# Kernel optimization log

Hardware: AMD Instinct MI355X
Metric: run time of the kernel (lower is better)

The kernel has to match this reference:

```python
import jax, jax.numpy as jnp
import numpy as np

B, N, P, C, H = 8, 512, 16, 512, 8
HD = C // H  # 64


def setup_inputs() -> dict:
    key = jax.random.key(0)
    k1, k2, k3, k4, k5 = jax.random.split(key, 5)
    x = jax.random.normal(k1, (B, N, P, C), dtype=jnp.float32)
    # binary observation mask; force slot 0 valid so masked mean never divides by 0
    mask = (jax.random.uniform(k2, (B, N, P)) > 0.3).astype(jnp.float32)
    mask = mask.at[:, :, 0].set(1.0)
    lens = jax.random.randint(k3, (B,), 1, N)
    lens_mask = jnp.ones((B, N), dtype=jnp.float32)
    # parameters (torch Linear stored as [in, out] here; qkv_bias=False, proj has bias)
    Wqkv = jax.random.normal(k4, (C, 3 * C), dtype=jnp.float32) * (1.0 / np.sqrt(C))
    Wproj = jax.random.normal(k5, (C, C), dtype=jnp.float32) * (1.0 / np.sqrt(C))
    bproj = jnp.zeros((C,), dtype=jnp.float32)
    return {"x": x, "mask": mask, "lens": lens, "lens_mask": lens_mask,
            "Wqkv": Wqkv, "Wproj": Wproj, "bproj": bproj}


def reference(x, mask, lens, lens_mask, Wqkv, Wproj, bproj):
    # lens / lens_mask are unused by the original forward
    b, n, p, c = x.shape
    h, hd = H, c // H
    qkv = jnp.einsum('bnpc,cd->bnpd', x, Wqkv).reshape(b, n, p, 3, h, hd)
    # q: take P-slot 0                       -> [B,H,N,hd]
    q = qkv[:, :, 0, 0].transpose(0, 2, 1, 3)
    # k: masked mean over P                  -> [B,H,N,hd]
    m = mask[..., None, None]                      # [B,N,P,1,1]
    k = (jnp.where(m > 0, qkv[:, :, :, 1], 0.0).sum(axis=2) / m.sum(axis=2))
    k = k.transpose(0, 2, 1, 3)
    # v: pack P into channel dim             -> [B,H,N,hd*P]
    v = qkv[:, :, :, 2].transpose(0, 3, 1, 4, 2).reshape(b, h, n, hd * p)
    # SDPA over N (scale by 1/sqrt(head_dim of q))
    scale = 1.0 / np.sqrt(hd)
    attn = jax.nn.softmax(jnp.einsum('bhnd,bhmd->bhnm', q, k) * scale, axis=-1)
    out = jnp.einsum('bhnm,bhme->bhne', attn, v)            # [B,H,N,hd*P]
    # unpack P back out                       -> [B,N,P,C]
    out = out.reshape(b, h, n, hd, p).transpose(0, 2, 4, 1, 3).reshape(b, n, p, c)
    return out @ Wproj + bproj
```

## Files before the change

### kernel.cpp

```cpp
#include <hip/hip_runtime.h>

typedef _Float16 f16;
typedef __attribute__((ext_vector_type(8))) _Float16 half8;
typedef __attribute__((ext_vector_type(2))) _Float16 half2v;
typedef __attribute__((ext_vector_type(4))) float float4v;

#define MODE_QK 0
#define MODE_V 1
#define MODE_PV 2
#define MODE_PROJ 3


__device__ __forceinline__ void gload16(const f16* g, f16* l) {
    __builtin_amdgcn_global_load_lds(
        (const __attribute__((address_space(1))) void*)g,
        (__attribute__((address_space(3))) void*)l, 16, 0, 0);
}

__global__ __launch_bounds__(256) void prep_kernel(
    const float* __restrict__ x, const float* __restrict__ mask,
    const float* __restrict__ Wqkv, const float* __restrict__ Wproj,
    f16* __restrict__ xf, f16* __restrict__ xmean,
    f16* __restrict__ WT, f16* __restrict__ WpT)
{
    if (blockIdx.x >= 4096) {
        int idx = (blockIdx.x - 4096) * 256 + threadIdx.x;
        if (idx < 1536 * 512) {
            int d = idx >> 9, c = idx & 511;
            WT[idx] = (f16)Wqkv[c * 1536 + d];
        } else {
            int i2 = idx - 1536 * 512;
            int d = i2 >> 9, c = i2 & 511;
            WpT[i2] = (f16)Wproj[c * 512 + d];
        }
        return;
    }
    int bn = blockIdx.x;
    int t = threadIdx.x;
    const float* xrow = x + (size_t)bn * 16 * 512;
    const float* mrow = mask + (size_t)bn * 16;
    float msum = 0.f;
    #pragma unroll
    for (int p = 0; p < 16; p++) msum += mrow[p];
    int c = t * 2;
    float a0 = 0.f, a1 = 0.f;
    #pragma unroll
    for (int p = 0; p < 16; p++) {
        float2 v = *(const float2*)(xrow + p * 512 + c);
        float m = mrow[p];
        a0 += m * v.x; a1 += m * v.y;
        half2v h; h[0] = (f16)v.x; h[1] = (f16)v.y;
        *(half2v*)(xf + (size_t)bn * 16 * 512 + p * 512 + c) = h;
    }
    float inv = 1.f / msum;
    half2v hm; hm[0] = (f16)(a0 * inv); hm[1] = (f16)(a1 * inv);
    *(half2v*)(xmean + (size_t)bn * 512 + c) = hm;
}

template<int MODE>
__global__ __launch_bounds__(256) void gemm128(
    const f16* __restrict__ pA, const f16* __restrict__ pA2,
    const f16* __restrict__ pB,
    f16* __restrict__ outa, f16* __restrict__ outb,
    float* __restrict__ outf, const float* __restrict__ bias)
{
    __shared__ __align__(16) f16 sm[18432];
    const int t = threadIdx.x;
    const int lane = t & 63;
    const int w = t >> 6;
    const int wm = w & 1, wn = w >> 1;
    const int quad = lane >> 4, l15 = lane & 15;

    const int n0 = blockIdx.x * 128;
    const int m0 = blockIdx.y * 128;
    int vb = 0, vp = 0, z = 0;

    const f16* Abase; size_t sA;
    const f16* Bbase; size_t sB;
    if constexpr (MODE == MODE_QK) {
        if (n0 < 512) { Abase = pA;  sA = 8192; }
        else          { Abase = pA2; sA = 512;  }
        Bbase = pB; sB = 512;
    } else if constexpr (MODE == MODE_V) {
        z = blockIdx.z; vb = z >> 4; vp = z & 15;
        Abase = pA; sA = 512;
        Bbase = pB + ((size_t)vb * 512 * 16 + vp) * 512; sB = 8192;
    } else if constexpr (MODE == MODE_PV) {
        z = blockIdx.z;
        Abase = pA + (size_t)z * 512 * 512; sA = 512;
        Bbase = pB + (size_t)z * 1024 * 512; sB = 512;
    } else {
        Abase = pA; sA = 512;
        Bbase = pB; sB = 512;
    }

    const int rlo = (lane >> 2), kof = (lane & 3) * 8;
    const f16* ga0 = Abase + (size_t)(m0 + w * 16 + rlo) * sA + kof;
    const f16* ga1 = Abase + (size_t)(m0 + (w + 4) * 16 + rlo) * sA + kof;
    const f16* gb0 = Bbase + (size_t)(n0 + w * 16 + rlo) * sB + kof;
    const f16* gb1 = Bbase + (size_t)(n0 + (w + 4) * 16 + rlo) * sB + kof;

    float4v acc[4][4];
    #pragma unroll
    for (int i = 0; i < 4; i++)
        #pragma unroll
        for (int j = 0; j < 4; j++)
            acc[i][j] = (float4v){0.f, 0.f, 0.f, 0.f};

    {
        f16* d = sm;
        gload16(ga0, d + w * 512); gload16(ga1, d + (w + 4) * 512);
        gload16(gb0, d + 4096 + w * 512); gload16(gb1, d + 4096 + (w + 4) * 512);
        ga0 += 32; ga1 += 32; gb0 += 32; gb1 += 32;
    }
    int cur = 0;
    for (int kt = 0; kt < 16; kt++) {
        __syncthreads();
        if (kt < 15) {
            f16* d = sm + (cur ^ 1) * 8192;
            gload16(ga0, d + w * 512); gload16(ga1, d + (w + 4) * 512);
            gload16(gb0, d + 4096 + w * 512); gload16(gb1, d + 4096 + (w + 4) * 512);
            ga0 += 32; ga1 += 32; gb0 += 32; gb1 += 32;
        }
        const f16* Asr = sm + cur * 8192;
        const f16* Bsr = Asr + 4096;
        half8 af[4], bf[4];
        #pragma unroll
        for (int mi = 0; mi < 4; mi++)
            af[mi] = *(const half8*)&Asr[(wm * 64 + mi * 16 + l15) * 32 + quad * 8];
        #pragma unroll
        for (int ni = 0; ni < 4; ni++)
            bf[ni] = *(const half8*)&Bsr[(wn * 64 + ni * 16 + l15) * 32 + quad * 8];
        #pragma unroll
        for (int mi = 0; mi < 4; mi++)
            #pragma unroll
            for (int ni = 0; ni < 4; ni++)
                acc[mi][ni] = __builtin_amdgcn_mfma_f32_16x16x32_f16(
                    af[mi], bf[ni], acc[mi][ni], 0, 0, 0);
        cur ^= 1;
    }

    __syncthreads();

    if constexpr (MODE == MODE_PROJ) {
        float* pwf = (float*)sm + w * 2176;
        const int rr4 = lane >> 4, c4 = (lane & 15) * 4;
        float4v bb = *(const float4v*)&bias[n0 + wn * 64 + c4];
        #pragma unroll
        for (int c2 = 0; c2 < 2; c2++) {
            #pragma unroll
            for (int mh = 0; mh < 2; mh++) {
                int mi = c2 * 2 + mh;
                #pragma unroll
                for (int ni = 0; ni < 4; ni++)
                    #pragma unroll
                    for (int i = 0; i < 4; i++)
                        pwf[(mh * 16 + quad * 4 + i) * 68 + ni * 16 + l15] =
                            acc[mi][ni][i];
            }
            #pragma unroll
            for (int s = 0; s < 8; s++) {
                int r = s * 4 + rr4;
                float4v v = *(const float4v*)&pwf[r * 68 + c4];
                *(float4v*)&outf[(size_t)(m0 + wm * 64 + c2 * 32 + r) * 512 +
                                 n0 + wn * 64 + c4] = v + bb;
            }
        }
    } else {
        f16* pw = sm + w * 4608;
        #pragma unroll
        for (int mi = 0; mi < 4; mi++)
            #pragma unroll
            for (int ni = 0; ni < 4; ni++)
                #pragma unroll
                for (int i = 0; i < 4; i++)
                    pw[(mi * 16 + quad * 4 + i) * 72 + ni * 16 + l15] =
                        (f16)acc[mi][ni][i];
        const int rr8 = lane >> 3, c8 = (lane & 7) * 8;
        #pragma unroll
        for (int s = 0; s < 8; s++) {
            int r = s * 8 + rr8;
            half8 v = *(const half8*)&pw[r * 72 + c8];
            int gr = m0 + wm * 64 + r;
            int gc = n0 + wn * 64 + c8;
            if constexpr (MODE == MODE_QK) {
                int b = gr >> 9, n = gr & 511;
                if (gc < 512)
                    *(half8*)&outa[(((size_t)(b * 8 + (gc >> 6))) * 512 + n) * 64 + (gc & 63)] = v;
                else {
                    int jj = gc - 512;
                    *(half8*)&outb[(((size_t)(b * 8 + (jj >> 6))) * 512 + n) * 64 + (jj & 63)] = v;
                }
            } else if constexpr (MODE == MODE_V) {
                int h = gr >> 6, dd = gr & 63;
                *(half8*)&outa[(((size_t)(vb * 8 + h)) * 1024 + vp * 64 + dd) * 512 + gc] = v;
            } else {
                int p = gc >> 6, dd = gc & 63;
                int b = z >> 3, h = z & 7;
                *(half8*)&outa[((size_t)(b * 512 + gr) * 16 + p) * 512 + h * 64 + dd] = v;
            }
        }
    }
}

__global__ __launch_bounds__(256) void qk_softmax_kernel(
    const f16* __restrict__ q, const f16* __restrict__ k, f16* __restrict__ Pout)
{
    __shared__ __align__(16) f16 sm[16896];
    const int t = threadIdx.x;
    const int lane = t & 63, w = t >> 6;
    const int quad = lane >> 4, l15 = lane & 15;
    const int bh = blockIdx.y;
    const int n0 = blockIdx.x * 64;

    const f16* kbase = k + (size_t)bh * 512 * 64;
    const f16* qp = q + ((size_t)bh * 512 + n0 + w * 16 + l15) * 64 + quad * 8;
    half8 a0 = *(const half8*)qp;
    half8 a1 = *(const half8*)(qp + 32);

    float4v acc[32];
    #pragma unroll
    for (int f = 0; f < 32; f++) acc[f] = (float4v){0.f, 0.f, 0.f, 0.f};

    const int srow = lane >> 3, scol = lane & 7;
    #pragma unroll
    for (int c = 0; c < 4; c++) {
        __syncthreads();
        #pragma unroll
        for (int i = 0; i < 4; i++) {
            int ci2 = w * 4 + i;
            int row = ci2 * 8 + srow;
            gload16(kbase + c * 8192 + row * 64 + ((scol ^ (row & 7)) << 3),
                    sm + ci2 * 512 + lane * 8);
        }
        __syncthreads();
        #pragma unroll
        for (int fl = 0; fl < 8; fl++) {
            int row16 = fl * 16 + l15;
            int sw = row16 & 7;
            half8 b0 = *(const half8*)&sm[row16 * 64 + ((quad ^ sw) << 3)];
            half8 b1 = *(const half8*)&sm[row16 * 64 + (((quad + 4) ^ sw) << 3)];
            acc[c * 8 + fl] = __builtin_amdgcn_mfma_f32_16x16x32_f16(
                a0, b0, acc[c * 8 + fl], 0, 0, 0);
            acc[c * 8 + fl] = __builtin_amdgcn_mfma_f32_16x16x32_f16(
                a1, b1, acc[c * 8 + fl], 0, 0, 0);
        }
    }

    float mx0 = -3e38f, mx1 = -3e38f, mx2 = -3e38f, mx3 = -3e38f;
    #pragma unroll
    for (int f = 0; f < 32; f++) {
        mx0 = fmaxf(mx0, acc[f][0]); mx1 = fmaxf(mx1, acc[f][1]);
        mx2 = fmaxf(mx2, acc[f][2]); mx3 = fmaxf(mx3, acc[f][3]);
    }
    #pragma unroll
    for (int off = 1; off < 16; off <<= 1) {
        mx0 = fmaxf(mx0, __shfl_xor(mx0, off));
        mx1 = fmaxf(mx1, __shfl_xor(mx1, off));
        mx2 = fmaxf(mx2, __shfl_xor(mx2, off));
        mx3 = fmaxf(mx3, __shfl_xor(mx3, off));
    }
    float s0 = 0.f, s1 = 0.f, s2 = 0.f, s3 = 0.f;
    #pragma unroll
    for (int f = 0; f < 32; f++) {
        float e0 = __expf(0.125f * (acc[f][0] - mx0));
        float e1 = __expf(0.125f * (acc[f][1] - mx1));
        float e2 = __expf(0.125f * (acc[f][2] - mx2));
        float e3 = __expf(0.125f * (acc[f][3] - mx3));
        acc[f][0] = e0; acc[f][1] = e1; acc[f][2] = e2; acc[f][3] = e3;
        s0 += e0; s1 += e1; s2 += e2; s3 += e3;
    }
    #pragma unroll
    for (int off = 1; off < 16; off <<= 1) {
        s0 += __shfl_xor(s0, off);
        s1 += __shfl_xor(s1, off);
        s2 += __shfl_xor(s2, off);
        s3 += __shfl_xor(s3, off);
    }
    float r0 = 1.f / s0, r1 = 1.f / s1, r2 = 1.f / s2, r3 = 1.f / s3;

    __syncthreads();
    f16* pb = sm + w * 4224;
    const int rr = lane >> 2, cb = (lane & 3) * 64;
    #pragma unroll
    for (int cc = 0; cc < 2; cc++) {
        #pragma unroll
        for (int ff = 0; ff < 16; ff++) {
            int f = cc * 16 + ff;
            pb[(quad * 4 + 0) * 264 + ff * 16 + l15] = (f16)(acc[f][0] * r0);
            pb[(quad * 4 + 1) * 264 + ff * 16 + l15] = (f16)(acc[f][1] * r1);
            pb[(quad * 4 + 2) * 264 + ff * 16 + l15] = (f16)(acc[f][2] * r2);
            pb[(quad * 4 + 3) * 264 + ff * 16 + l15] = (f16)(acc[f][3] * r3);
        }
        size_t gb = ((size_t)bh * 512 + n0 + w * 16 + rr) * 512 + cc * 256 + cb;
        #pragma unroll
        for (int s = 0; s < 8; s++) {
            half8 v = *(const half8*)&pb[rr * 264 + cb + s * 8];
            *(half8*)&Pout[gb + s * 8] = v;
        }
    }
}

extern "C" void kernel_launch(void* const* d_in, const int* in_sizes, int n_in,
                              void* d_out, int out_size, void* d_ws, size_t ws_size,
                              hipStream_t stream)
{
    (void)in_sizes; (void)n_in; (void)out_size; (void)ws_size;
    const float* x     = (const float*)d_in[0];
    const float* mask  = (const float*)d_in[1];
    const float* Wqkv  = (const float*)d_in[4];
    const float* Wproj = (const float*)d_in[5];
    const float* bproj = (const float*)d_in[6];
    float* out = (float*)d_out;
    char* ws = (char*)d_ws;

    f16* xf16  = (f16*)(ws + 0);
    f16* vT    = (f16*)(ws + 67108864);
    f16* xmean = (f16*)(ws + 134217728);
    f16* WT    = (f16*)(ws + 138412032);
    f16* WpT   = (f16*)(ws + 139984896);
    f16* qb    = (f16*)(ws + 140509184);
    f16* kb    = (f16*)(ws + 144703488);
    f16* Pm    = (f16*)(ws + 148897792);
    f16* ypre  = xf16;

    prep_kernel<<<dim3(8192), dim3(256), 0, stream>>>(
        x, mask, Wqkv, Wproj, xf16, xmean, WT, WpT);
    gemm128<MODE_QK><<<dim3(8, 32), dim3(256), 0, stream>>>(
        xf16, xmean, WT, qb, kb, nullptr, nullptr);
    gemm128<MODE_V><<<dim3(4, 4, 128), dim3(256), 0, stream>>>(
        WT + 1024 * 512, nullptr, xf16, vT, nullptr, nullptr, nullptr);
    qk_softmax_kernel<<<dim3(8, 64), dim3(256), 0, stream>>>(qb, kb, Pm);
    gemm128<MODE_PV><<<dim3(8, 4, 64), dim3(256), 0, stream>>>(
        Pm, nullptr, vT, ypre, nullptr, nullptr, nullptr);
    gemm128<MODE_PROJ><<<dim3(4, 512), dim3(256), 0, stream>>>(
        ypre, nullptr, WpT, nullptr, nullptr, out, bproj);
}
```

Measured before the change: 438.6 us.

## Remap GEMM blocks per XCD, swizzle LDS tiles, shrink epilogue staging

Block indices in the GEMM and QK-softmax kernels are flattened to 1D and remapped so that consecutive logical tiles go to the same XCD chiplet. This aims to improve L2 reuse of shared A/B panels. The LDS tile layout gets an XOR swizzle on the k-offset, applied on both the global-to-LDS copy and the fragment reads, to cut bank conflicts. The epilogue staging is split into smaller chunks, which lowers shared memory from 36KB to 32KB to raise occupancy, at the cost of more passes through LDS.

```diff
diff --git a/kernel.cpp b/kernel.cpp
--- a/kernel.cpp
+++ b/kernel.cpp
@@ -57,23 +57,29 @@
     *(half2v*)(xmean + (size_t)bn * 512 + c) = hm;
 }
 
-template<int MODE>
+template<int MODE, int NXB, int NYB>
 __global__ __launch_bounds__(256) void gemm128(
     const f16* __restrict__ pA, const f16* __restrict__ pA2,
     const f16* __restrict__ pB,
     f16* __restrict__ outa, f16* __restrict__ outb,
     float* __restrict__ outf, const float* __restrict__ bias)
 {
-    __shared__ __align__(16) f16 sm[18432];
+    __shared__ __align__(16) f16 sm[16384];
     const int t = threadIdx.x;
     const int lane = t & 63;
     const int w = t >> 6;
     const int wm = w & 1, wn = w >> 1;
     const int quad = lane >> 4, l15 = lane & 15;
 
-    const int n0 = blockIdx.x * 128;
-    const int m0 = blockIdx.y * 128;
-    int vb = 0, vp = 0, z = 0;
+    const int chunk = (int)gridDim.x >> 3;
+    const int L = ((int)blockIdx.x & 7) * chunk + ((int)blockIdx.x >> 3);
+    const int xb = L & ((1 << NXB) - 1);
+    const int rest = L >> NXB;
+    const int yb = rest & ((1 << NYB) - 1);
+    const int z = rest >> NYB;
+    const int n0 = xb * 128;
+    const int m0 = yb * 128;
+    int vb = 0, vp = 0;
 
     const f16* Abase; size_t sA;
     const f16* Bbase; size_t sB;
@@ -82,11 +88,10 @@
         else          { Abase = pA2; sA = 512;  }
         Bbase = pB; sB = 512;
     } else if constexpr (MODE == MODE_V) {
-        z = blockIdx.z; vb = z >> 4; vp = z & 15;
+        vb = z >> 4; vp = z & 15;
         Abase = pA; sA = 512;
         Bbase = pB + ((size_t)vb * 512 * 16 + vp) * 512; sB = 8192;
     } else if constexpr (MODE == MODE_PV) {
-        z = blockIdx.z;
         Abase = pA + (size_t)z * 512 * 512; sA = 512;
         Bbase = pB + (size_t)z * 1024 * 512; sB = 512;
     } else {
@@ -94,7 +99,8 @@
         Bbase = pB; sB = 512;
     }
 
-    const int rlo = (lane >> 2), kof = (lane & 3) * 8;
+    const int rlo = (lane >> 2);
+    const int kof = (((lane & 3) ^ ((rlo >> 1) & 3)) * 8);
     const f16* ga0 = Abase + (size_t)(m0 + w * 16 + rlo) * sA + kof;
     const f16* ga1 = Abase + (size_t)(m0 + (w + 4) * 16 + rlo) * sA + kof;
     const f16* gb0 = Bbase + (size_t)(n0 + w * 16 + rlo) * sB + kof;
@@ -113,6 +119,7 @@
         gload16(gb0, d + 4096 + w * 512); gload16(gb1, d + 4096 + (w + 4) * 512);
         ga0 += 32; ga1 += 32; gb0 += 32; gb1 += 32;
     }
+    const int sws = (l15 >> 1) & 3;
     int cur = 0;
     for (int kt = 0; kt < 16; kt++) {
         __syncthreads();
@@ -127,10 +134,12 @@
         half8 af[4], bf[4];
         #pragma unroll
         for (int mi = 0; mi < 4; mi++)
-            af[mi] = *(const half8*)&Asr[(wm * 64 + mi * 16 + l15) * 32 + quad * 8];
+            af[mi] = *(const half8*)&Asr[(wm * 64 + mi * 16 + l15) * 32 +
+                                         ((quad ^ sws) * 8)];
         #pragma unroll
         for (int ni = 0; ni < 4; ni++)
-            bf[ni] = *(const half8*)&Bsr[(wn * 64 + ni * 16 + l15) * 32 + quad * 8];
+            bf[ni] = *(const half8*)&Bsr[(wn * 64 + ni * 16 + l15) * 32 +
+                                         ((quad ^ sws) * 8)];
         #pragma unroll
         for (int mi = 0; mi < 4; mi++)
             #pragma unroll
@@ -143,61 +152,61 @@
     __syncthreads();
 
     if constexpr (MODE == MODE_PROJ) {
-        float* pwf = (float*)sm + w * 2176;
-        const int rr4 = lane >> 4, c4 = (lane & 15) * 4;
-        float4v bb = *(const float4v*)&bias[n0 + wn * 64 + c4];
-        #pragma unroll
-        for (int c2 = 0; c2 < 2; c2++) {
+        float* pwf = (float*)sm + w * 1088;
+        const int rr4 = lane >> 4, c4c = (lane & 15) * 4;
+        float4v bb = *(const float4v*)&bias[n0 + wn * 64 + c4c];
+        #pragma unroll
+        for (int mi = 0; mi < 4; mi++) {
+            #pragma unroll
+            for (int ni = 0; ni < 4; ni++)
+                #pragma unroll
+                for (int i = 0; i < 4; i++)
+                    pwf[(quad * 4 + i) * 68 + ni * 16 + l15] = acc[mi][ni][i];
+            #pragma unroll
+            for (int s = 0; s < 4; s++) {
+                int r = s * 4 + rr4;
+                float4v v = *(const float4v*)&pwf[r * 68 + c4c];
+                *(float4v*)&outf[(size_t)(m0 + wm * 64 + mi * 16 + r) * 512 +
+                                 n0 + wn * 64 + c4c] = v + bb;
+            }
+        }
+    } else {
+        f16* pw = sm + w * 2304;
+        const int rr8 = lane >> 3, c8 = (lane & 7) * 8;
+        #pragma unroll
+        for (int hf = 0; hf < 2; hf++) {
             #pragma unroll
             for (int mh = 0; mh < 2; mh++) {
-                int mi = c2 * 2 + mh;
+                int mi = hf * 2 + mh;
                 #pragma unroll
                 for (int ni = 0; ni < 4; ni++)
                     #pragma unroll
                     for (int i = 0; i < 4; i++)
-                        pwf[(mh * 16 + quad * 4 + i) * 68 + ni * 16 + l15] =
-                            acc[mi][ni][i];
+                        pw[(mh * 16 + quad * 4 + i) * 72 + ni * 16 + l15] =
+                            (f16)acc[mi][ni][i];
             }
             #pragma unroll
-            for (int s = 0; s < 8; s++) {
-                int r = s * 4 + rr4;
-                float4v v = *(const float4v*)&pwf[r * 68 + c4];
-                *(float4v*)&outf[(size_t)(m0 + wm * 64 + c2 * 32 + r) * 512 +
-                                 n0 + wn * 64 + c4] = v + bb;
-            }
-        }
-    } else {
-        f16* pw = sm + w * 4608;
-        #pragma unroll
-        for (int mi = 0; mi < 4; mi++)
-            #pragma unroll
-            for (int ni = 0; ni < 4; ni++)
-                #pragma unroll
-                for (int i = 0; i < 4; i++)
-                    pw[(mi * 16 + quad * 4 + i) * 72 + ni * 16 + l15] =
-                        (f16)acc[mi][ni][i];
-        const int rr8 = lane >> 3, c8 = (lane & 7) * 8;
-        #pragma unroll
-        for (int s = 0; s < 8; s++) {
-            int r = s * 8 + rr8;
-            half8 v = *(const half8*)&pw[r * 72 + c8];
-            int gr = m0 + wm * 64 + r;
-            int gc = n0 + wn * 64 + c8;
-            if constexpr (MODE == MODE_QK) {
-                int b = gr >> 9, n = gr & 511;
-                if (gc < 512)
-                    *(half8*)&outa[(((size_t)(b * 8 + (gc >> 6))) * 512 + n) * 64 + (gc & 63)] = v;
-                else {
-                    int jj = gc - 512;
-                    *(half8*)&outb[(((size_t)(b * 8 + (jj >> 6))) * 512 + n) * 64 + (jj & 63)] = v;
+            for (int s = 0; s < 4; s++) {
+                int r = s * 8 + rr8;
+                half8 v = *(const half8*)&pw[r * 72 + c8];
+                int gr = m0 + wm * 64 + hf * 32 + r;
+                int gc = n0 + wn * 64 + c8;
+                if constexpr (MODE == MODE_QK) {
+                    int b = gr >> 9, n = gr & 511;
+                    if (gc < 512)
+                        *(half8*)&outa[(((size_t)(b * 8 + (gc >> 6))) * 512 + n) * 64 + (gc & 63)] = v;
+                    else {
+                        int jj = gc - 512;
+                        *(half8*)&outb[(((size_t)(b * 8 + (jj >> 6))) * 512 + n) * 64 + (jj & 63)] = v;
+                    }
+                } else if constexpr (MODE == MODE_V) {
+                    int h = gr >> 6, dd = gr & 63;
+                    *(half8*)&outa[(((size_t)(vb * 8 + h)) * 1024 + vp * 64 + dd) * 512 + gc] = v;
+                } else {
+                    int p = gc >> 6, dd = gc & 63;
+                    int b = z >> 3, h = z & 7;
+                    *(half8*)&outa[((size_t)(b * 512 + gr) * 16 + p) * 512 + h * 64 + dd] = v;
                 }
-            } else if constexpr (MODE == MODE_V) {
-                int h = gr >> 6, dd = gr & 63;
-                *(half8*)&outa[(((size_t)(vb * 8 + h)) * 1024 + vp * 64 + dd) * 512 + gc] = v;
-            } else {
-                int p = gc >> 6, dd = gc & 63;
-                int b = z >> 3, h = z & 7;
-                *(half8*)&outa[((size_t)(b * 512 + gr) * 16 + p) * 512 + h * 64 + dd] = v;
             }
         }
     }
@@ -210,8 +219,9 @@
     const int t = threadIdx.x;
     const int lane = t & 63, w = t >> 6;
     const int quad = lane >> 4, l15 = lane & 15;
-    const int bh = blockIdx.y;
-    const int n0 = blockIdx.x * 64;
+    const int L = ((int)blockIdx.x & 7) * 64 + ((int)blockIdx.x >> 3);
+    const int bh = L >> 3;
+    const int n0 = (L & 7) * 64;
 
     const f16* kbase = k + (size_t)bh * 512 * 64;
     const f16* qp = q + ((size_t)bh * 512 + n0 + w * 16 + l15) * 64 + quad * 8;
@@ -326,13 +336,13 @@
 
     prep_kernel<<<dim3(8192), dim3(256), 0, stream>>>(
         x, mask, Wqkv, Wproj, xf16, xmean, WT, WpT);
-    gemm128<MODE_QK><<<dim3(8, 32), dim3(256), 0, stream>>>(
+    gemm128<MODE_QK, 3, 5><<<dim3(256), dim3(256), 0, stream>>>(
         xf16, xmean, WT, qb, kb, nullptr, nullptr);
-    gemm128<MODE_V><<<dim3(4, 4, 128), dim3(256), 0, stream>>>(
+    gemm128<MODE_V, 2, 2><<<dim3(2048), dim3(256), 0, stream>>>(
         WT + 1024 * 512, nullptr, xf16, vT, nullptr, nullptr, nullptr);
-    qk_softmax_kernel<<<dim3(8, 64), dim3(256), 0, stream>>>(qb, kb, Pm);
-    gemm128<MODE_PV><<<dim3(8, 4, 64), dim3(256), 0, stream>>>(
+    qk_softmax_kernel<<<dim3(512), dim3(256), 0, stream>>>(qb, kb, Pm);
+    gemm128<MODE_PV, 3, 2><<<dim3(2048), dim3(256), 0, stream>>>(
         Pm, nullptr, vT, ypre, nullptr, nullptr, nullptr);
-    gemm128<MODE_PROJ><<<dim3(4, 512), dim3(256), 0, stream>>>(
+    gemm128<MODE_PROJ, 2, 9><<<dim3(2048), dim3(256), 0, stream>>>(
         ypre, nullptr, WpT, nullptr, nullptr, out, bproj);
 }
```

Result: faster. 421.9 us (-3.8%).
